# Optimization experiments

Measured on AMD Instinct MI355X. Metric: run time of the kernel, lower is better.

## Reference

```python
import jax, jax.numpy as jnp
import numpy as np

RAY_START, RAY_END, BOX_SIZE = 0.0, 1.0, 2.0
EPS = 1e-10


def grid_sample_bilinear(img, grid):
    """Replicates F.grid_sample(mode='bilinear', padding_mode='zeros', align_corners=True).
    img: [N, F, H, W]; grid: [N, P, 2] with (x, y) in [-1, 1] (x indexes W, y indexes H).
    Returns [N, F, P]."""
    H, W = img.shape[2], img.shape[3]
    x = (grid[..., 0] + 1.0) * 0.5 * (W - 1)  # [N, P]
    y = (grid[..., 1] + 1.0) * 0.5 * (H - 1)
    x0 = jnp.floor(x).astype(jnp.int32)
    y0 = jnp.floor(y).astype(jnp.int32)
    x1, y1 = x0 + 1, y0 + 1
    wx = x - x0.astype(x.dtype)
    wy = y - y0.astype(y.dtype)

    def gather(ix, iy):
        valid = ((ix >= 0) & (ix < W) & (iy >= 0) & (iy < H)).astype(img.dtype)
        ixc = jnp.clip(ix, 0, W - 1)
        iyc = jnp.clip(iy, 0, H - 1)
        v = jax.vmap(lambda im, jx, jy: im[:, jy, jx])(img, ixc, iyc)  # [N, F, P]
        return v * valid[:, None, :]

    return (gather(x0, y0) * ((1 - wx) * (1 - wy))[:, None, :]
            + gather(x1, y0) * (wx * (1 - wy))[:, None, :]
            + gather(x0, y1) * ((1 - wx) * wy)[:, None, :]
            + gather(x1, y1) * (wx * wy)[:, None, :])


def setup_inputs() -> dict:
    key = jax.random.key(0)
    ks = jax.random.split(key, 6)
    B, R, N, F, HP, HID = 2, 4096, 48, 32, 256, 64
    planes = jax.random.normal(ks[0], (B, 3, F, HP, HP), jnp.float32)
    ray_origins = jax.random.normal(ks[1], (B, R, 3), jnp.float32) * 0.05
    rd = jax.random.normal(ks[2], (B, R, 3), jnp.float32)
    ray_directions = rd / jnp.linalg.norm(rd, axis=-1, keepdims=True)
    jitter = jax.random.uniform(ks[3], (B, R, N, 1), jnp.float32)
    W1 = jax.random.normal(ks[4], (F, HID), jnp.float32) * 0.1
    b1 = jnp.zeros((HID,), jnp.float32)
    W2 = jax.random.normal(ks[5], (HID, 4), jnp.float32) * 0.1
    b2 = jnp.zeros((4,), jnp.float32)
    return dict(planes=planes, ray_origins=ray_origins, ray_directions=ray_directions,
                jitter=jitter, W1=W1, b1=b1, W2=W2, b2=b2)


def reference(planes, ray_origins, ray_directions, jitter, W1, b1, W2, b2):
    B, R, N, _ = jitter.shape
    F_, HP, WP = planes.shape[2], planes.shape[3], planes.shape[4]
    P = R * N

    # sample_stratified over normalized s in [0, 1], jittered (EG3D style)
    steps = jnp.arange(N, dtype=jnp.float32) / (N - 1)          # [N]
    s_delta = 1.0 / (N - 1)
    sdist = steps.reshape(1, 1, N, 1) + jitter * s_delta         # [B, R, N, 1]
    tdist = sdist * RAY_END + (1.0 - sdist) * RAY_START          # s_to_t

    # world-space sample coordinates -> tri-plane lookup
    coords = ray_origins[:, :, None, :] + tdist * ray_directions[:, :, None, :]  # [B,R,N,3]
    coords = coords.reshape(B, P, 3) / (BOX_SIZE / 2.0)
    c2d = jnp.stack([coords[..., (0, 1)], coords[..., (0, 2)], coords[..., (1, 2)]],
                    axis=1).reshape(B * 3, P, 2)
    feats = grid_sample_bilinear(planes.reshape(B * 3, F_, HP, WP), c2d)  # [B*3, F, P]
    feats = feats.reshape(B, 3, F_, P).transpose(0, 1, 3, 2)              # [B, 3, P, F]

    # OSGDecoder-style MLP: mean over planes, Linear -> softplus -> Linear
    x = feats.mean(axis=1)                      # [B, P, F]
    h = jax.nn.softplus(x @ W1 + b1)            # [B, P, HID]
    o = h @ W2 + b2                             # [B, P, 4]
    sigma = o[..., :1].reshape(B, R, N, 1)
    rgb = (jax.nn.sigmoid(o[..., 1:]) * 1.002 - 0.001).reshape(B, R, N, 3)

    # ClassicalRayMarcher (clamp_mode='softplus', cut_quantile=0, use_inf_depth=True)
    deltas = sdist[:, :, 1:] - sdist[:, :, :-1]
    deltas = jnp.concatenate([deltas, jnp.full_like(deltas[:, :, :1], 1e10)], axis=2)
    dens = jax.nn.softplus(sigma)
    alphas = 1.0 - jnp.exp(-deltas * dens)                     # [B, R, N, 1]
    T = jnp.cumprod(1.0 - alphas + EPS, axis=2)
    T = jnp.concatenate([jnp.ones_like(T[:, :, :1]), T], axis=2)  # [B, R, N+1, 1]
    final_transmittance = T[:, :, -1, 0]                       # [B, R]
    weights = alphas * T[:, :, :-1]                            # [B, R, N, 1]
    rgb_final = jnp.sum(weights * rgb, axis=2)                 # [B, R, 3]
    depth = jnp.sum(weights * sdist, axis=2)                   # [B, R, 1]
    return rgb_final, depth, weights.sum(axis=2), final_transmittance
```

## Files before the change

### kernel.cpp

```cpp
#include <hip/hip_runtime.h>
#include <hip/hip_fp16.h>
#include <math.h>

#define BATCH 2
#define RAYS  4096
#define NS    48
#define FEAT  32
#define HP    256
#define HID   64
#define NRAY  (BATCH*RAYS)
#define NSAMP (NRAY*NS)
#define S_DELTA (1.0f/47.0f)
#define PSZ   (HP*HP*FEAT)

typedef unsigned short u16;
typedef __attribute__((ext_vector_type(8))) _Float16 half8;
typedef __attribute__((ext_vector_type(4))) float facc4;

__device__ __forceinline__ float softplus_f(float t) {
    float e = __expf(-fabsf(t));
    return fmaxf(t, 0.0f) + __logf(1.0f + e);
}
__device__ __forceinline__ float sigmoid_f(float t) {
    return 1.0f / (1.0f + __expf(-t));
}

__global__ __launch_bounds__(256)
void prep_kernel(const float* __restrict__ planes,
                 const float* __restrict__ W1,
                 const float* __restrict__ W2,
                 u16* __restrict__ pT,
                 u16* __restrict__ W1F,
                 u16* __restrict__ W2F) {
    int idx = blockIdx.x * 256 + threadIdx.x;
    const int total = BATCH * 3 * HP * HP;
    if (idx < total) {
        int xy = idx % (HP * HP);
        int bp = idx / (HP * HP);
        const float* src = planes + (size_t)bp * FEAT * HP * HP + xy;
        unsigned o16[16];
        #pragma unroll
        for (int k = 0; k < 16; ++k) {
            unsigned lo = __half_as_ushort(__float2half_rn(src[(size_t)(2*k)   * HP*HP]));
            unsigned hi = __half_as_ushort(__float2half_rn(src[(size_t)(2*k+1) * HP*HP]));
            o16[k] = lo | (hi << 16);
        }
        uint4* dst = (uint4*)(pT + (size_t)idx * FEAT);
        #pragma unroll
        for (int q = 0; q < 4; ++q)
            dst[q] = make_uint4(o16[4*q], o16[4*q+1], o16[4*q+2], o16[4*q+3]);
    } else {
        int r = idx - total;
        #pragma unroll
        for (int i = 0; i < 8; ++i) {
            int e = r * 8 + i;
            int nt = e >> 9, ll = (e >> 3) & 63, ii = e & 7;
            int k = ((ll >> 4) << 3) + ii;
            int nn = (nt << 4) + (ll & 15);
            W1F[e] = __half_as_ushort(__float2half_rn(W1[k * HID + nn] * (1.f/3.f)));
        }
        if (r < 128) {
            #pragma unroll
            for (int i = 0; i < 8; ++i) {
                int e = r * 8 + i;
                int kk = e >> 9, ll = (e >> 3) & 63, ii = e & 7;
                int k = kk * 32 + ((ll >> 4) << 3) + ii;
                int nn = ll & 15;
                W2F[e] = (nn < 4) ? __half_as_ushort(__float2half_rn(W2[k * 4 + nn]))
                                  : (u16)0;
            }
        }
    }
}

__device__ __forceinline__ void plane_addr(float gx, float gy, int fc8, unsigned pofs,
                                           unsigned* __restrict__ offs,
                                           float* __restrict__ wts) {
    float px = fmaf(gx, 127.5f, 127.5f);
    float py = fmaf(gy, 127.5f, 127.5f);
    float fx = floorf(px), fy = floorf(py);
    float wx = px - fx, wy = py - fy;
    int x0 = (int)fx, y0 = (int)fy;
    int x1 = x0 + 1, y1 = y0 + 1;
    bool vx0 = (unsigned)x0 < HP, vx1 = (unsigned)x1 < HP;
    bool vy0 = (unsigned)y0 < HP, vy1 = (unsigned)y1 < HP;
    int cx0 = min(max(x0, 0), HP-1), cx1 = min(max(x1, 0), HP-1);
    int cy0 = min(max(y0, 0), HP-1), cy1 = min(max(y1, 0), HP-1);
    unsigned a00 = (unsigned)(cy0 * HP + cx0) * FEAT + fc8 + pofs;
    unsigned dxe = (unsigned)(cx1 - cx0) * FEAT;
    unsigned dye = (unsigned)(cy1 - cy0) * (HP * FEAT);
    offs[0] = a00;
    offs[1] = a00 + dxe;
    offs[2] = a00 + dye;
    offs[3] = a00 + dye + dxe;
    wts[0] = (vx0 && vy0) ? (1.f-wx)*(1.f-wy) : 0.f;
    wts[1] = (vx1 && vy0) ? wx*(1.f-wy)       : 0.f;
    wts[2] = (vx0 && vy1) ? (1.f-wx)*wy       : 0.f;
    wts[3] = (vx1 && vy1) ? wx*wy             : 0.f;
}

__global__ __launch_bounds__(192, 4)
void render_mfma(const u16* __restrict__ pT,
                 const float* __restrict__ rayo,
                 const float* __restrict__ rayd,
                 const float* __restrict__ jitter,
                 const u16* __restrict__ W1F,
                 const u16* __restrict__ W2F,
                 const float* __restrict__ b1,
                 const float* __restrict__ b2,
                 float* __restrict__ out) {
    __shared__ __align__(16) u16 hlds[3][1024];
    __shared__ __align__(16) float4 s_smp[48];
    __shared__ float s_sd[48];

    const int t = threadIdx.x;
    const int w = t >> 6;
    const int l = t & 63;
    const int c = l & 15;
    const int g = l >> 4;
    const int ray = blockIdx.x;
    const int ls = w * 16 + c;
    const int s  = ray * NS + ls;
    const int b  = ray >> 12;

    const float jit = jitter[s];
    const float sd = fmaf((float)ls, S_DELTA, jit * S_DELTA);
    const float ox = rayo[ray*3+0], oy = rayo[ray*3+1], oz = rayo[ray*3+2];
    const float dx = rayd[ray*3+0], dy = rayd[ray*3+1], dz = rayd[ray*3+2];
    const float cxv = fmaf(sd, dx, ox);
    const float cyv = fmaf(sd, dy, oy);
    const float czv = fmaf(sd, dz, oz);

    const int fc8 = g * 8;
    unsigned offs[12];
    float wts[12];
    plane_addr(cxv, cyv, fc8, 0u,          offs + 0, wts + 0);
    plane_addr(cxv, czv, fc8, (unsigned)PSZ,     offs + 4, wts + 4);
    plane_addr(cyv, czv, fc8, (unsigned)(2*PSZ), offs + 8, wts + 8);

    const u16* pbase = pT + (size_t)b * 3 * PSZ;
    uint4 dat[12];
    #pragma unroll
    for (int i = 0; i < 12; ++i)
        dat[i] = *(const uint4*)(pbase + offs[i]);

    __half2 a0[4], a1[4], a2[4];
    #pragma unroll
    for (int i = 0; i < 4; ++i) {
        a0[i] = __float2half2_rn(0.f);
        a1[i] = __float2half2_rn(0.f);
        a2[i] = __float2half2_rn(0.f);
    }
    #pragma unroll
    for (int q = 0; q < 4; ++q) {
        union { uint4 u; __half2 h[4]; } d0, d1, d2;
        d0.u = dat[q]; d1.u = dat[4+q]; d2.u = dat[8+q];
        __half2 w0 = __float2half2_rn(wts[q]);
        __half2 w1 = __float2half2_rn(wts[4+q]);
        __half2 w2 = __float2half2_rn(wts[8+q]);
        #pragma unroll
        for (int j = 0; j < 4; ++j) {
            a0[j] = __hfma2(d0.h[j], w0, a0[j]);
            a1[j] = __hfma2(d1.h[j], w1, a1[j]);
            a2[j] = __hfma2(d2.h[j], w2, a2[j]);
        }
    }

    union { __half2 h[4]; half8 v; } A;
    #pragma unroll
    for (int i = 0; i < 4; ++i)
        A.h[i] = __hadd2(__hadd2(a0[i], a1[i]), a2[i]);

    facc4 H[4];
    #pragma unroll
    for (int nt = 0; nt < 4; ++nt) {
        const float bb = b1[nt * 16 + c];
        facc4 Cb = {bb, bb, bb, bb};
        union { uint4 q; half8 v; } B;
        B.q = *(const uint4*)(W1F + (size_t)(nt * 64 + l) * 8);
        H[nt] = __builtin_amdgcn_mfma_f32_16x16x32_f16(A.v, B.v, Cb, 0, 0, 0);
    }

    char* lb = (char*)&hlds[w][0];
    #pragma unroll
    for (int nt = 0; nt < 4; ++nt) {
        #pragma unroll
        for (int r = 0; r < 4; ++r) {
            const int row = g * 4 + r;
            const float hv = softplus_f(H[nt][r]);
            const int off = row * 128 + ((((nt * 16 + c) * 2)) ^ ((row & 7) << 4));
            *(u16*)(lb + off) = __half_as_ushort(__float2half_rn(hv));
        }
    }

    const float bb2 = b2[c & 3];
    facc4 O = {bb2, bb2, bb2, bb2};
    #pragma unroll
    for (int kk = 0; kk < 2; ++kk) {
        union { uint4 q; half8 v; } A2;
        const int off = c * 128 + ((kk * 64 + g * 16) ^ ((c & 7) << 4));
        A2.q = *(const uint4*)(lb + off);
        union { uint4 q; half8 v; } B2;
        B2.q = *(const uint4*)(W2F + (size_t)(kk * 64 + l) * 8);
        O = __builtin_amdgcn_mfma_f32_16x16x32_f16(A2.v, B2.v, O, 0, 0, 0);
    }

    if (c < 4) {
        #pragma unroll
        for (int r = 0; r < 4; ++r) {
            const int li = w * 16 + g * 4 + r;
            const float o = O[r];
            const float val = (c == 0) ? softplus_f(o)
                                       : (sigmoid_f(o) * 1.002f - 0.001f);
            ((float*)&s_smp[li])[c] = val;
        }
    }
    if (g == 0) s_sd[ls] = sd;
    __syncthreads();

    if (w == 0) {
        const bool valid = l < NS;
        float4 v = make_float4(0.f, 0.f, 0.f, 0.f);
        float sdc = 0.f;
        if (valid) { v = s_smp[l]; sdc = s_sd[l]; }
        float sdn = __shfl_down(sdc, 1);

        float alpha = 0.f, lg = 0.f;
        if (valid) {
            float delta = (l < NS - 1) ? (sdn - sdc) : 1e10f;
            float tt = __expf(-delta * v.x);
            alpha = 1.0f - tt;
            lg = __logf(tt + 1e-10f);
        }
        float sacc = lg;
        #pragma unroll
        for (int off = 1; off < 64; off <<= 1) {
            float u = __shfl_up(sacc, off);
            if (l >= off) sacc += u;
        }
        float finalLog = __shfl(sacc, NS - 1);
        float T   = __expf(sacc - lg);
        float wgt = valid ? alpha * T : 0.f;

        float rf = wgt * v.y, gf = wgt * v.z, bf = wgt * v.w;
        float dep = wgt * sdc, wsum = wgt;
        #pragma unroll
        for (int off = 32; off; off >>= 1) {
            rf   += __shfl_xor(rf, off);
            gf   += __shfl_xor(gf, off);
            bf   += __shfl_xor(bf, off);
            dep  += __shfl_xor(dep, off);
            wsum += __shfl_xor(wsum, off);
        }
        if (l == 0) {
            out[ray * 3 + 0] = rf;
            out[ray * 3 + 1] = gf;
            out[ray * 3 + 2] = bf;
            out[NRAY * 3 + ray] = dep;
            out[NRAY * 4 + ray] = wsum;
            out[NRAY * 5 + ray] = __expf(finalLog);
        }
    }
}

__global__ __launch_bounds__(192)
void render_fused(const float* __restrict__ pl,
                  const float* __restrict__ rayo,
                  const float* __restrict__ rayd,
                  const float* __restrict__ jitter,
                  const float* __restrict__ W1, const float* __restrict__ b1,
                  const float* __restrict__ W2, const float* __restrict__ b2,
                  float* __restrict__ out) {
    __shared__ float4 smpb[192];
    __shared__ float  sdsb[192];
    int tid = threadIdx.x;
    int lr  = tid / NS;
    int n   = tid - lr * NS;
    int ray = blockIdx.x * 4 + lr;
    int b   = ray >> 12;

    float jit = jitter[ray * NS + n];
    float sd  = (float)n * S_DELTA + jit * S_DELTA;
    float ox = rayo[ray*3+0], oy = rayo[ray*3+1], oz = rayo[ray*3+2];
    float dx = rayd[ray*3+0], dy = rayd[ray*3+1], dz = rayd[ray*3+2];
    float cx = fmaf(sd, dx, ox), cy = fmaf(sd, dy, oy), cz = fmaf(sd, dz, oz);

    float xv[32];
    #pragma unroll
    for (int i = 0; i < 32; ++i) xv[i] = 0.f;
    const size_t psz = (size_t)HP * HP * FEAT;
    const float* base = pl + (size_t)b * 3 * psz;
    float gxs[3] = {cx, cx, cy}, gys[3] = {cy, cz, cz};
    for (int p = 0; p < 3; ++p) {
        float px = (gxs[p] + 1.0f) * 0.5f * (float)(HP - 1);
        float py = (gys[p] + 1.0f) * 0.5f * (float)(HP - 1);
        float fx = floorf(px), fy = floorf(py);
        float wx = px - fx, wy = py - fy;
        int x0 = (int)fx, y0 = (int)fy, x1 = x0 + 1, y1 = y0 + 1;
        const float* pb = base + p * psz;
        float ws[4] = {(1.f-wx)*(1.f-wy), wx*(1.f-wy), (1.f-wx)*wy, wx*wy};
        int xs[4] = {x0, x1, x0, x1}, ys[4] = {y0, y0, y1, y1};
        for (int q = 0; q < 4; ++q) {
            if ((unsigned)xs[q] < HP && (unsigned)ys[q] < HP) {
                const float* pp = pb + (size_t)ys[q] * HP + xs[q];
                #pragma unroll
                for (int f = 0; f < 32; ++f)
                    xv[f] = fmaf(ws[q], pp[(size_t)f * HP * HP], xv[f]);
            }
        }
    }
    #pragma unroll
    for (int i = 0; i < 32; ++i) xv[i] *= (1.f/3.f);

    float o0 = b2[0], o1 = b2[1], o2 = b2[2], o3 = b2[3];
    #pragma unroll
    for (int j = 0; j < HID; ++j) {
        float hj = b1[j];
        #pragma unroll
        for (int f = 0; f < FEAT; ++f) hj = fmaf(xv[f], W1[f * HID + j], hj);
        hj = softplus_f(hj);
        o0 = fmaf(hj, W2[j*4+0], o0);
        o1 = fmaf(hj, W2[j*4+1], o1);
        o2 = fmaf(hj, W2[j*4+2], o2);
        o3 = fmaf(hj, W2[j*4+3], o3);
    }
    smpb[tid] = make_float4(softplus_f(o0),
                            sigmoid_f(o1) * 1.002f - 0.001f,
                            sigmoid_f(o2) * 1.002f - 0.001f,
                            sigmoid_f(o3) * 1.002f - 0.001f);
    sdsb[tid] = sd;
    __syncthreads();

    if (tid < 4) {
        int rray = blockIdx.x * 4 + tid;
        const float4* sp  = &smpb[tid * NS];
        const float*  sdp = &sdsb[tid * NS];
        float T = 1.0f, rf = 0.f, gf = 0.f, bfv = 0.f, dep = 0.f, wsum = 0.f;
        for (int m = 0; m < NS; ++m) {
            float4 vv = sp[m];
            float sdc = sdp[m];
            float delta = (m < NS - 1) ? (sdp[m+1] - sdc) : 1e10f;
            float alpha = 1.0f - __expf(-delta * vv.x);
            float wq = alpha * T;
            rf = fmaf(wq, vv.y, rf);
            gf = fmaf(wq, vv.z, gf);
            bfv = fmaf(wq, vv.w, bfv);
            dep = fmaf(wq, sdc, dep);
            wsum += wq;
            T *= (1.0f - alpha + 1e-10f);
        }
        out[rray*3+0] = rf;
        out[rray*3+1] = gf;
        out[rray*3+2] = bfv;
        out[NRAY*3 + rray] = dep;
        out[NRAY*4 + rray] = wsum;
        out[NRAY*5 + rray] = T;
    }
}

extern "C" void kernel_launch(void* const* d_in, const int* in_sizes, int n_in,
                              void* d_out, int out_size, void* d_ws, size_t ws_size,
                              hipStream_t stream) {
    const float* planes = (const float*)d_in[0];
    const float* rayo   = (const float*)d_in[1];
    const float* rayd   = (const float*)d_in[2];
    const float* jitter = (const float*)d_in[3];
    const float* W1     = (const float*)d_in[4];
    const float* b1     = (const float*)d_in[5];
    const float* W2     = (const float*)d_in[6];
    const float* b2     = (const float*)d_in[7];
    float* out = (float*)d_out;

    const size_t pT_bytes = (size_t)BATCH * 3 * HP * HP * FEAT * 2;
    const size_t w1f_off  = pT_bytes;
    const size_t w2f_off  = w1f_off + (size_t)FEAT * HID * 2;
    const size_t need     = w2f_off + (size_t)HID * 16 * 2;

    if (ws_size >= need) {
        char* ws = (char*)d_ws;
        u16* pT  = (u16*)ws;
        u16* W1F = (u16*)(ws + w1f_off);
        u16* W2F = (u16*)(ws + w2f_off);
        const int tgrid = BATCH * 3 * HP * HP / 256 + 1;
        hipLaunchKernelGGL(prep_kernel, dim3(tgrid), dim3(256), 0, stream,
                           planes, W1, W2, pT, W1F, W2F);
        hipLaunchKernelGGL(render_mfma, dim3(NRAY), dim3(192), 0, stream,
                           pT, rayo, rayd, jitter, W1F, W2F, b1, b2, out);
    } else {
        hipLaunchKernelGGL(render_fused, dim3(NRAY / 4), dim3(192), 0, stream,
                           planes, rayo, rayd, jitter, W1, b1, W2, b2, out);
    }
}
```

Baseline: 58.04 us.

## Switch MLP to 32x32x16 MFMA and process two rays per block

Each block now handles two rays (96 samples), with each wave covering 32 samples using 32x32x16 MFMA tiles instead of 16x16x32. Each lane gathers 16 features per corner (two 8-wide loads) instead of 8, and the weight prep layouts for W1/W2 are reordered to match the new fragment format. The aim is fewer blocks, better MFMA utilisation and fewer wasted output columns in the second layer. The cost is more registers per thread (16-wide accumulators, doubled gather buffers) and more LDS, which may lower occupancy.

Result: slower. 69.42 us (+19.6%).

```diff
diff --git a/kernel.cpp b/kernel.cpp
--- a/kernel.cpp
+++ b/kernel.cpp
@@ -14,8 +14,8 @@
 #define PSZ   (HP*HP*FEAT)
 
 typedef unsigned short u16;
-typedef __attribute__((ext_vector_type(8))) _Float16 half8;
-typedef __attribute__((ext_vector_type(4))) float facc4;
+typedef __attribute__((ext_vector_type(8)))  _Float16 half8;
+typedef __attribute__((ext_vector_type(16))) float    f32x16;
 
 __device__ __forceinline__ float softplus_f(float t) {
     float e = __expf(-fabsf(t));
@@ -54,21 +54,20 @@
         #pragma unroll
         for (int i = 0; i < 8; ++i) {
             int e = r * 8 + i;
-            int nt = e >> 9, ll = (e >> 3) & 63, ii = e & 7;
-            int k = ((ll >> 4) << 3) + ii;
-            int nn = (nt << 4) + (ll & 15);
+            int tile = e >> 9, ll = (e >> 3) & 63, ii = e & 7;
+            int nt = tile >> 1, kk = tile & 1;
+            int k  = kk * 16 + ((ll >> 5) << 3) + ii;
+            int nn = nt * 32 + (ll & 31);
             W1F[e] = __half_as_ushort(__float2half_rn(W1[k * HID + nn] * (1.f/3.f)));
         }
-        if (r < 128) {
-            #pragma unroll
-            for (int i = 0; i < 8; ++i) {
-                int e = r * 8 + i;
-                int kk = e >> 9, ll = (e >> 3) & 63, ii = e & 7;
-                int k = kk * 32 + ((ll >> 4) << 3) + ii;
-                int nn = ll & 15;
-                W2F[e] = (nn < 4) ? __half_as_ushort(__float2half_rn(W2[k * 4 + nn]))
-                                  : (u16)0;
-            }
+        #pragma unroll
+        for (int i = 0; i < 8; ++i) {
+            int e = r * 8 + i;
+            int kk2 = e >> 9, ll = (e >> 3) & 63, ii = e & 7;
+            int k   = kk2 * 16 + ((ll >> 5) << 3) + ii;
+            int col = ll & 31;
+            W2F[e] = (col < 4) ? __half_as_ushort(__float2half_rn(W2[k * 4 + col]))
+                               : (u16)0;
         }
     }
 }
@@ -109,120 +108,131 @@
                  const float* __restrict__ b1,
                  const float* __restrict__ b2,
                  float* __restrict__ out) {
-    __shared__ __align__(16) u16 hlds[3][1024];
-    __shared__ __align__(16) float4 s_smp[48];
-    __shared__ float s_sd[48];
+    __shared__ __align__(16) u16 hlds[3][2048];
+    __shared__ __align__(16) float4 s_smp[96];
+    __shared__ float s_sd[96];
 
     const int t = threadIdx.x;
     const int w = t >> 6;
     const int l = t & 63;
-    const int c = l & 15;
-    const int g = l >> 4;
-    const int ray = blockIdx.x;
-    const int ls = w * 16 + c;
-    const int s  = ray * NS + ls;
+    const int c = l & 31;
+    const int h = l >> 5;
+    const int R0 = blockIdx.x * 2;
+    const int ls = w * 32 + c;
+    const int rl = (ls >= NS) ? 1 : 0;
+    const int n  = ls - NS * rl;
+    const int ray = R0 + rl;
+    const int s  = ray * NS + n;
     const int b  = ray >> 12;
 
     const float jit = jitter[s];
-    const float sd = fmaf((float)ls, S_DELTA, jit * S_DELTA);
+    const float sd = fmaf((float)n, S_DELTA, jit * S_DELTA);
     const float ox = rayo[ray*3+0], oy = rayo[ray*3+1], oz = rayo[ray*3+2];
     const float dx = rayd[ray*3+0], dy = rayd[ray*3+1], dz = rayd[ray*3+2];
     const float cxv = fmaf(sd, dx, ox);
     const float cyv = fmaf(sd, dy, oy);
     const float czv = fmaf(sd, dz, oz);
 
-    const int fc8 = g * 8;
+    const int fc8 = h * 8;
     unsigned offs[12];
     float wts[12];
-    plane_addr(cxv, cyv, fc8, 0u,          offs + 0, wts + 0);
+    plane_addr(cxv, cyv, fc8, 0u,                offs + 0, wts + 0);
     plane_addr(cxv, czv, fc8, (unsigned)PSZ,     offs + 4, wts + 4);
     plane_addr(cyv, czv, fc8, (unsigned)(2*PSZ), offs + 8, wts + 8);
 
     const u16* pbase = pT + (size_t)b * 3 * PSZ;
-    uint4 dat[12];
-    #pragma unroll
-    for (int i = 0; i < 12; ++i)
-        dat[i] = *(const uint4*)(pbase + offs[i]);
-
-    __half2 a0[4], a1[4], a2[4];
+
+    __half2 acc0[3][4], acc1[3][4];
+    #pragma unroll
+    for (int p = 0; p < 3; ++p)
+        #pragma unroll
+        for (int i = 0; i < 4; ++i) {
+            acc0[p][i] = __float2half2_rn(0.f);
+            acc1[p][i] = __float2half2_rn(0.f);
+        }
+    #pragma unroll
+    for (int q = 0; q < 4; ++q) {
+        #pragma unroll
+        for (int p = 0; p < 3; ++p) {
+            const u16* cp = pbase + offs[4*p + q];
+            union { uint4 u; __half2 hh[4]; } d0, d1;
+            d0.u = *(const uint4*)cp;
+            d1.u = *(const uint4*)(cp + 16);
+            __half2 wv = __float2half2_rn(wts[4*p + q]);
+            #pragma unroll
+            for (int j = 0; j < 4; ++j) {
+                acc0[p][j] = __hfma2(d0.hh[j], wv, acc0[p][j]);
+                acc1[p][j] = __hfma2(d1.hh[j], wv, acc1[p][j]);
+            }
+        }
+    }
+    union { __half2 hh[4]; half8 v; } A0, A1;
     #pragma unroll
     for (int i = 0; i < 4; ++i) {
-        a0[i] = __float2half2_rn(0.f);
-        a1[i] = __float2half2_rn(0.f);
-        a2[i] = __float2half2_rn(0.f);
-    }
-    #pragma unroll
-    for (int q = 0; q < 4; ++q) {
-        union { uint4 u; __half2 h[4]; } d0, d1, d2;
-        d0.u = dat[q]; d1.u = dat[4+q]; d2.u = dat[8+q];
-        __half2 w0 = __float2half2_rn(wts[q]);
-        __half2 w1 = __float2half2_rn(wts[4+q]);
-        __half2 w2 = __float2half2_rn(wts[8+q]);
-        #pragma unroll
-        for (int j = 0; j < 4; ++j) {
-            a0[j] = __hfma2(d0.h[j], w0, a0[j]);
-            a1[j] = __hfma2(d1.h[j], w1, a1[j]);
-            a2[j] = __hfma2(d2.h[j], w2, a2[j]);
-        }
-    }
-
-    union { __half2 h[4]; half8 v; } A;
-    #pragma unroll
-    for (int i = 0; i < 4; ++i)
-        A.h[i] = __hadd2(__hadd2(a0[i], a1[i]), a2[i]);
-
-    facc4 H[4];
-    #pragma unroll
-    for (int nt = 0; nt < 4; ++nt) {
-        const float bb = b1[nt * 16 + c];
-        facc4 Cb = {bb, bb, bb, bb};
-        union { uint4 q; half8 v; } B;
-        B.q = *(const uint4*)(W1F + (size_t)(nt * 64 + l) * 8);
-        H[nt] = __builtin_amdgcn_mfma_f32_16x16x32_f16(A.v, B.v, Cb, 0, 0, 0);
+        A0.hh[i] = __hadd2(__hadd2(acc0[0][i], acc0[1][i]), acc0[2][i]);
+        A1.hh[i] = __hadd2(__hadd2(acc1[0][i], acc1[1][i]), acc1[2][i]);
+    }
+
+    f32x16 H[2];
+    #pragma unroll
+    for (int nt = 0; nt < 2; ++nt) {
+        const float bb = b1[nt * 32 + c];
+        f32x16 Cb;
+        #pragma unroll
+        for (int i = 0; i < 16; ++i) Cb[i] = bb;
+        union { uint4 q; half8 v; } B0, B1;
+        B0.q = *(const uint4*)(W1F + (size_t)((nt*2+0) * 64 + l) * 8);
+        B1.q = *(const uint4*)(W1F + (size_t)((nt*2+1) * 64 + l) * 8);
+        H[nt] = __builtin_amdgcn_mfma_f32_32x32x16_f16(A0.v, B0.v, Cb,    0, 0, 0);
+        H[nt] = __builtin_amdgcn_mfma_f32_32x32x16_f16(A1.v, B1.v, H[nt], 0, 0, 0);
     }
 
     char* lb = (char*)&hlds[w][0];
     #pragma unroll
-    for (int nt = 0; nt < 4; ++nt) {
-        #pragma unroll
-        for (int r = 0; r < 4; ++r) {
-            const int row = g * 4 + r;
-            const float hv = softplus_f(H[nt][r]);
-            const int off = row * 128 + ((((nt * 16 + c) * 2)) ^ ((row & 7) << 4));
+    for (int nt = 0; nt < 2; ++nt) {
+        #pragma unroll
+        for (int reg = 0; reg < 16; ++reg) {
+            const int row = (reg & 3) + 8 * (reg >> 2) + 4 * h;
+            const float hv = softplus_f(H[nt][reg]);
+            const int off = row * 128 + ((nt * 64 + c * 2) ^ ((row & 7) << 4));
             *(u16*)(lb + off) = __half_as_ushort(__float2half_rn(hv));
         }
     }
 
     const float bb2 = b2[c & 3];
-    facc4 O = {bb2, bb2, bb2, bb2};
-    #pragma unroll
-    for (int kk = 0; kk < 2; ++kk) {
+    f32x16 O;
+    #pragma unroll
+    for (int i = 0; i < 16; ++i) O[i] = bb2;
+    #pragma unroll
+    for (int kk2 = 0; kk2 < 4; ++kk2) {
         union { uint4 q; half8 v; } A2;
-        const int off = c * 128 + ((kk * 64 + g * 16) ^ ((c & 7) << 4));
+        const int off = c * 128 + ((kk2 * 32 + h * 16) ^ ((c & 7) << 4));
         A2.q = *(const uint4*)(lb + off);
         union { uint4 q; half8 v; } B2;
-        B2.q = *(const uint4*)(W2F + (size_t)(kk * 64 + l) * 8);
-        O = __builtin_amdgcn_mfma_f32_16x16x32_f16(A2.v, B2.v, O, 0, 0, 0);
+        B2.q = *(const uint4*)(W2F + (size_t)(kk2 * 64 + l) * 8);
+        O = __builtin_amdgcn_mfma_f32_32x32x16_f16(A2.v, B2.v, O, 0, 0, 0);
     }
 
     if (c < 4) {
         #pragma unroll
-        for (int r = 0; r < 4; ++r) {
-            const int li = w * 16 + g * 4 + r;
-            const float o = O[r];
+        for (int reg = 0; reg < 16; ++reg) {
+            const int row = (reg & 3) + 8 * (reg >> 2) + 4 * h;
+            const int li = w * 32 + row;
+            const float o = O[reg];
             const float val = (c == 0) ? softplus_f(o)
                                        : (sigmoid_f(o) * 1.002f - 0.001f);
             ((float*)&s_smp[li])[c] = val;
         }
     }
-    if (g == 0) s_sd[ls] = sd;
+    if (h == 0) s_sd[ls] = sd;
     __syncthreads();
 
-    if (w == 0) {
+    if (w < 2) {
+        const int rray = R0 + w;
         const bool valid = l < NS;
         float4 v = make_float4(0.f, 0.f, 0.f, 0.f);
         float sdc = 0.f;
-        if (valid) { v = s_smp[l]; sdc = s_sd[l]; }
+        if (valid) { v = s_smp[w * NS + l]; sdc = s_sd[w * NS + l]; }
         float sdn = __shfl_down(sdc, 1);
 
         float alpha = 0.f, lg = 0.f;
@@ -253,12 +263,12 @@
             wsum += __shfl_xor(wsum, off);
         }
         if (l == 0) {
-            out[ray * 3 + 0] = rf;
-            out[ray * 3 + 1] = gf;
-            out[ray * 3 + 2] = bf;
-            out[NRAY * 3 + ray] = dep;
-            out[NRAY * 4 + ray] = wsum;
-            out[NRAY * 5 + ray] = __expf(finalLog);
+            out[rray * 3 + 0] = rf;
+            out[rray * 3 + 1] = gf;
+            out[rray * 3 + 2] = bf;
+            out[NRAY * 3 + rray] = dep;
+            out[NRAY * 4 + rray] = wsum;
+            out[NRAY * 5 + rray] = __expf(finalLog);
         }
     }
 }
@@ -373,8 +383,8 @@
 
     const size_t pT_bytes = (size_t)BATCH * 3 * HP * HP * FEAT * 2;
     const size_t w1f_off  = pT_bytes;
-    const size_t w2f_off  = w1f_off + (size_t)FEAT * HID * 2;
-    const size_t need     = w2f_off + (size_t)HID * 16 * 2;
+    const size_t w2f_off  = w1f_off + 2048 * 2;
+    const size_t need     = w2f_off + 2048 * 2;
 
     if (ws_size >= need) {
         char* ws = (char*)d_ws;
@@ -384,7 +394,7 @@
         const int tgrid = BATCH * 3 * HP * HP / 256 + 1;
         hipLaunchKernelGGL(prep_kernel, dim3(tgrid), dim3(256), 0, stream,
                            planes, W1, W2, pT, W1F, W2F);
-        hipLaunchKernelGGL(render_mfma, dim3(NRAY), dim3(192), 0, stream,
+        hipLaunchKernelGGL(render_mfma, dim3(NRAY / 2), dim3(192), 0, stream,
                            pT, rayo, rayd, jitter, W1F, W2F, b1, b2, out);
     } else {
         hipLaunchKernelGGL(render_fused, dim3(NRAY / 4), dim3(192), 0, stream,
```

## Process four rays per block and hoist MLP weight loads out of ray loop

Applied to the files above, without the earlier changes.

The render kernel now loops over four rays per block instead of one, launching a quarter as many blocks. W1/W2 fragments and biases are loaded once into registers and reused across rays, and the sample result buffers are double-buffered so the next ray's writes do not race with the compositing wave. This aims to cut per-block launch and weight-load overhead, at the cost of fewer blocks for latency hiding and less up-front issue of plane gathers.

New measurement: 71.14 us. 22.6% more time.

```diff
diff --git a/kernel.cpp b/kernel.cpp
--- a/kernel.cpp
+++ b/kernel.cpp
@@ -12,6 +12,7 @@
 #define NSAMP (NRAY*NS)
 #define S_DELTA (1.0f/47.0f)
 #define PSZ   (HP*HP*FEAT)
+#define RPB   4
 
 typedef unsigned short u16;
 typedef __attribute__((ext_vector_type(8))) _Float16 half8;
@@ -110,155 +111,164 @@
                  const float* __restrict__ b2,
                  float* __restrict__ out) {
     __shared__ __align__(16) u16 hlds[3][1024];
-    __shared__ __align__(16) float4 s_smp[48];
-    __shared__ float s_sd[48];
+    __shared__ __align__(16) float4 s_smp[2][48];
+    __shared__ float s_sd[2][48];
 
     const int t = threadIdx.x;
     const int w = t >> 6;
     const int l = t & 63;
     const int c = l & 15;
     const int g = l >> 4;
-    const int ray = blockIdx.x;
+    const int R0 = blockIdx.x * RPB;
     const int ls = w * 16 + c;
-    const int s  = ray * NS + ls;
-    const int b  = ray >> 12;
-
-    const float jit = jitter[s];
-    const float sd = fmaf((float)ls, S_DELTA, jit * S_DELTA);
-    const float ox = rayo[ray*3+0], oy = rayo[ray*3+1], oz = rayo[ray*3+2];
-    const float dx = rayd[ray*3+0], dy = rayd[ray*3+1], dz = rayd[ray*3+2];
-    const float cxv = fmaf(sd, dx, ox);
-    const float cyv = fmaf(sd, dy, oy);
-    const float czv = fmaf(sd, dz, oz);
-
+    const int b  = R0 >> 12;
     const int fc8 = g * 8;
-    unsigned offs[12];
-    float wts[12];
-    plane_addr(cxv, cyv, fc8, 0u,          offs + 0, wts + 0);
-    plane_addr(cxv, czv, fc8, (unsigned)PSZ,     offs + 4, wts + 4);
-    plane_addr(cyv, czv, fc8, (unsigned)(2*PSZ), offs + 8, wts + 8);
-
     const u16* pbase = pT + (size_t)b * 3 * PSZ;
-    uint4 dat[12];
-    #pragma unroll
-    for (int i = 0; i < 12; ++i)
-        dat[i] = *(const uint4*)(pbase + offs[i]);
-
-    __half2 a0[4], a1[4], a2[4];
-    #pragma unroll
-    for (int i = 0; i < 4; ++i) {
-        a0[i] = __float2half2_rn(0.f);
-        a1[i] = __float2half2_rn(0.f);
-        a2[i] = __float2half2_rn(0.f);
-    }
-    #pragma unroll
-    for (int q = 0; q < 4; ++q) {
-        union { uint4 u; __half2 h[4]; } d0, d1, d2;
-        d0.u = dat[q]; d1.u = dat[4+q]; d2.u = dat[8+q];
-        __half2 w0 = __float2half2_rn(wts[q]);
-        __half2 w1 = __float2half2_rn(wts[4+q]);
-        __half2 w2 = __float2half2_rn(wts[8+q]);
-        #pragma unroll
-        for (int j = 0; j < 4; ++j) {
-            a0[j] = __hfma2(d0.h[j], w0, a0[j]);
-            a1[j] = __hfma2(d1.h[j], w1, a1[j]);
-            a2[j] = __hfma2(d2.h[j], w2, a2[j]);
-        }
-    }
-
-    union { __half2 h[4]; half8 v; } A;
-    #pragma unroll
-    for (int i = 0; i < 4; ++i)
-        A.h[i] = __hadd2(__hadd2(a0[i], a1[i]), a2[i]);
-
-    facc4 H[4];
-    #pragma unroll
-    for (int nt = 0; nt < 4; ++nt) {
-        const float bb = b1[nt * 16 + c];
-        facc4 Cb = {bb, bb, bb, bb};
-        union { uint4 q; half8 v; } B;
-        B.q = *(const uint4*)(W1F + (size_t)(nt * 64 + l) * 8);
-        H[nt] = __builtin_amdgcn_mfma_f32_16x16x32_f16(A.v, B.v, Cb, 0, 0, 0);
-    }
-
     char* lb = (char*)&hlds[w][0];
-    #pragma unroll
-    for (int nt = 0; nt < 4; ++nt) {
-        #pragma unroll
-        for (int r = 0; r < 4; ++r) {
-            const int row = g * 4 + r;
-            const float hv = softplus_f(H[nt][r]);
-            const int off = row * 128 + ((((nt * 16 + c) * 2)) ^ ((row & 7) << 4));
-            *(u16*)(lb + off) = __half_as_ushort(__float2half_rn(hv));
-        }
-    }
-
+
+    uint4 B1q[4], B2q[2];
+    #pragma unroll
+    for (int nt = 0; nt < 4; ++nt)
+        B1q[nt] = *(const uint4*)(W1F + (size_t)(nt * 64 + l) * 8);
+    #pragma unroll
+    for (int kk = 0; kk < 2; ++kk)
+        B2q[kk] = *(const uint4*)(W2F + (size_t)(kk * 64 + l) * 8);
+    float bb1[4];
+    #pragma unroll
+    for (int nt = 0; nt < 4; ++nt) bb1[nt] = b1[nt * 16 + c];
     const float bb2 = b2[c & 3];
-    facc4 O = {bb2, bb2, bb2, bb2};
-    #pragma unroll
-    for (int kk = 0; kk < 2; ++kk) {
-        union { uint4 q; half8 v; } A2;
-        const int off = c * 128 + ((kk * 64 + g * 16) ^ ((c & 7) << 4));
-        A2.q = *(const uint4*)(lb + off);
-        union { uint4 q; half8 v; } B2;
-        B2.q = *(const uint4*)(W2F + (size_t)(kk * 64 + l) * 8);
-        O = __builtin_amdgcn_mfma_f32_16x16x32_f16(A2.v, B2.v, O, 0, 0, 0);
-    }
-
-    if (c < 4) {
-        #pragma unroll
-        for (int r = 0; r < 4; ++r) {
-            const int li = w * 16 + g * 4 + r;
-            const float o = O[r];
-            const float val = (c == 0) ? softplus_f(o)
-                                       : (sigmoid_f(o) * 1.002f - 0.001f);
-            ((float*)&s_smp[li])[c] = val;
-        }
-    }
-    if (g == 0) s_sd[ls] = sd;
-    __syncthreads();
-
-    if (w == 0) {
-        const bool valid = l < NS;
-        float4 v = make_float4(0.f, 0.f, 0.f, 0.f);
-        float sdc = 0.f;
-        if (valid) { v = s_smp[l]; sdc = s_sd[l]; }
-        float sdn = __shfl_down(sdc, 1);
-
-        float alpha = 0.f, lg = 0.f;
-        if (valid) {
-            float delta = (l < NS - 1) ? (sdn - sdc) : 1e10f;
-            float tt = __expf(-delta * v.x);
-            alpha = 1.0f - tt;
-            lg = __logf(tt + 1e-10f);
-        }
-        float sacc = lg;
-        #pragma unroll
-        for (int off = 1; off < 64; off <<= 1) {
-            float u = __shfl_up(sacc, off);
-            if (l >= off) sacc += u;
-        }
-        float finalLog = __shfl(sacc, NS - 1);
-        float T   = __expf(sacc - lg);
-        float wgt = valid ? alpha * T : 0.f;
-
-        float rf = wgt * v.y, gf = wgt * v.z, bf = wgt * v.w;
-        float dep = wgt * sdc, wsum = wgt;
-        #pragma unroll
-        for (int off = 32; off; off >>= 1) {
-            rf   += __shfl_xor(rf, off);
-            gf   += __shfl_xor(gf, off);
-            bf   += __shfl_xor(bf, off);
-            dep  += __shfl_xor(dep, off);
-            wsum += __shfl_xor(wsum, off);
-        }
-        if (l == 0) {
-            out[ray * 3 + 0] = rf;
-            out[ray * 3 + 1] = gf;
-            out[ray * 3 + 2] = bf;
-            out[NRAY * 3 + ray] = dep;
-            out[NRAY * 4 + ray] = wsum;
-            out[NRAY * 5 + ray] = __expf(finalLog);
+
+    for (int it = 0; it < RPB; ++it) {
+        const int ray = R0 + it;
+        const int s   = ray * NS + ls;
+        const int bi  = it & 1;
+
+        const float jit = jitter[s];
+        const float sd = fmaf((float)ls, S_DELTA, jit * S_DELTA);
+        const float ox = rayo[ray*3+0], oy = rayo[ray*3+1], oz = rayo[ray*3+2];
+        const float dx = rayd[ray*3+0], dy = rayd[ray*3+1], dz = rayd[ray*3+2];
+        const float cxv = fmaf(sd, dx, ox);
+        const float cyv = fmaf(sd, dy, oy);
+        const float czv = fmaf(sd, dz, oz);
+
+        unsigned offs[12];
+        float wts[12];
+        plane_addr(cxv, cyv, fc8, 0u,                offs + 0, wts + 0);
+        plane_addr(cxv, czv, fc8, (unsigned)PSZ,     offs + 4, wts + 4);
+        plane_addr(cyv, czv, fc8, (unsigned)(2*PSZ), offs + 8, wts + 8);
+
+        __half2 a0[4], a1[4], a2[4];
+        #pragma unroll
+        for (int i = 0; i < 4; ++i) {
+            a0[i] = __float2half2_rn(0.f);
+            a1[i] = __float2half2_rn(0.f);
+            a2[i] = __float2half2_rn(0.f);
+        }
+        #pragma unroll
+        for (int q = 0; q < 4; ++q) {
+            union { uint4 u; __half2 h[4]; } d0, d1, d2;
+            d0.u = *(const uint4*)(pbase + offs[q]);
+            d1.u = *(const uint4*)(pbase + offs[4+q]);
+            d2.u = *(const uint4*)(pbase + offs[8+q]);
+            __half2 w0 = __float2half2_rn(wts[q]);
+            __half2 w1 = __float2half2_rn(wts[4+q]);
+            __half2 w2 = __float2half2_rn(wts[8+q]);
+            #pragma unroll
+            for (int j = 0; j < 4; ++j) {
+                a0[j] = __hfma2(d0.h[j], w0, a0[j]);
+                a1[j] = __hfma2(d1.h[j], w1, a1[j]);
+                a2[j] = __hfma2(d2.h[j], w2, a2[j]);
+            }
+        }
+        union { __half2 h[4]; half8 v; } A;
+        #pragma unroll
+        for (int i = 0; i < 4; ++i)
+            A.h[i] = __hadd2(__hadd2(a0[i], a1[i]), a2[i]);
+
+        facc4 H[4];
+        #pragma unroll
+        for (int nt = 0; nt < 4; ++nt) {
+            facc4 Cb = {bb1[nt], bb1[nt], bb1[nt], bb1[nt]};
+            union { uint4 q; half8 v; } B; B.q = B1q[nt];
+            H[nt] = __builtin_amdgcn_mfma_f32_16x16x32_f16(A.v, B.v, Cb, 0, 0, 0);
+        }
+
+        #pragma unroll
+        for (int nt = 0; nt < 4; ++nt) {
+            #pragma unroll
+            for (int r = 0; r < 4; ++r) {
+                const int row = g * 4 + r;
+                const float hv = softplus_f(H[nt][r]);
+                const int off = row * 128 + ((((nt * 16 + c) * 2)) ^ ((row & 7) << 4));
+                *(u16*)(lb + off) = __half_as_ushort(__float2half_rn(hv));
+            }
+        }
+
+        facc4 O = {bb2, bb2, bb2, bb2};
+        #pragma unroll
+        for (int kk = 0; kk < 2; ++kk) {
+            union { uint4 q; half8 v; } A2;
+            const int off = c * 128 + ((kk * 64 + g * 16) ^ ((c & 7) << 4));
+            A2.q = *(const uint4*)(lb + off);
+            union { uint4 q; half8 v; } B2; B2.q = B2q[kk];
+            O = __builtin_amdgcn_mfma_f32_16x16x32_f16(A2.v, B2.v, O, 0, 0, 0);
+        }
+
+        if (c < 4) {
+            #pragma unroll
+            for (int r = 0; r < 4; ++r) {
+                const int li = w * 16 + g * 4 + r;
+                const float o = O[r];
+                const float val = (c == 0) ? softplus_f(o)
+                                           : (sigmoid_f(o) * 1.002f - 0.001f);
+                ((float*)&s_smp[bi][li])[c] = val;
+            }
+        }
+        if (g == 0) s_sd[bi][ls] = sd;
+        __syncthreads();
+
+        if (w == 0) {
+            const bool valid = l < NS;
+            float4 v = make_float4(0.f, 0.f, 0.f, 0.f);
+            float sdc = 0.f;
+            if (valid) { v = s_smp[bi][l]; sdc = s_sd[bi][l]; }
+            float sdn = __shfl_down(sdc, 1);
+
+            float alpha = 0.f, lg = 0.f;
+            if (valid) {
+                float delta = (l < NS - 1) ? (sdn - sdc) : 1e10f;
+                float tt = __expf(-delta * v.x);
+                alpha = 1.0f - tt;
+                lg = __logf(tt + 1e-10f);
+            }
+            float sacc = lg;
+            #pragma unroll
+            for (int off = 1; off < 64; off <<= 1) {
+                float u = __shfl_up(sacc, off);
+                if (l >= off) sacc += u;
+            }
+            float finalLog = __shfl(sacc, NS - 1);
+            float T   = __expf(sacc - lg);
+            float wgt = valid ? alpha * T : 0.f;
+
+            float rf = wgt * v.y, gf = wgt * v.z, bf = wgt * v.w;
+            float dep = wgt * sdc, wsum = wgt;
+            #pragma unroll
+            for (int off = 32; off; off >>= 1) {
+                rf   += __shfl_xor(rf, off);
+                gf   += __shfl_xor(gf, off);
+                bf   += __shfl_xor(bf, off);
+                dep  += __shfl_xor(dep, off);
+                wsum += __shfl_xor(wsum, off);
+            }
+            if (l == 0) {
+                out[ray * 3 + 0] = rf;
+                out[ray * 3 + 1] = gf;
+                out[ray * 3 + 2] = bf;
+                out[NRAY * 3 + ray] = dep;
+                out[NRAY * 4 + ray] = wsum;
+                out[NRAY * 5 + ray] = __expf(finalLog);
+            }
         }
     }
 }
@@ -384,7 +394,7 @@
         const int tgrid = BATCH * 3 * HP * HP / 256 + 1;
         hipLaunchKernelGGL(prep_kernel, dim3(tgrid), dim3(256), 0, stream,
                            planes, W1, W2, pT, W1F, W2F);
-        hipLaunchKernelGGL(render_mfma, dim3(NRAY), dim3(192), 0, stream,
+        hipLaunchKernelGGL(render_mfma, dim3(NRAY / RPB), dim3(192), 0, stream,
                            pT, rayo, rayd, jitter, W1F, W2F, b1, b2, out);
     } else {
         hipLaunchKernelGGL(render_fused, dim3(NRAY / 4), dim3(192), 0, stream,
```
